# Optimization experiments

Measured on AMD Instinct MI355X. Metric: run time of the kernel, lower is better.

Reference implementation:

```python
import jax, jax.numpy as jnp
import numpy as np

N_NODES = 40000
N_EDGES = 640000
D_IN = 128
D_HID = 128
D_OUT = 128


def _glorot(key, shape):
    fan_in, fan_out = shape[1], shape[0]
    lim = np.sqrt(6.0 / (fan_in + fan_out))
    return jax.random.uniform(key, shape, jnp.float32, -lim, lim)


def setup_inputs() -> dict:
    key = jax.random.key(0)
    ks = jax.random.split(key, 8)
    x = jax.random.normal(ks[0], (N_NODES, D_IN), jnp.float32)
    edge_index = jax.random.randint(ks[1], (2, N_EDGES), 0, N_NODES, jnp.int64)
    return {
        "x": x,
        "edge_index": edge_index,
        # layer 1 (SAGEConv -> hidden): lin_l (neighbor branch, with bias), lin_r (root, no bias)
        "W1_l": _glorot(ks[2], (D_HID, D_IN)),
        "b1_l": jnp.zeros((D_HID,), jnp.float32),
        "W1_r": _glorot(ks[3], (D_HID, D_IN)),
        # layer 2 (SAGEConv -> out)
        "W2_l": _glorot(ks[4], (D_OUT, D_HID)),
        "b2_l": jnp.zeros((D_OUT,), jnp.float32),
        "W2_r": _glorot(ks[5], (D_OUT, D_HID)),
    }


def _sage_conv(x, src, dst, W_l, b_l, W_r, n_nodes):
    # mean aggregation of source features at destination nodes
    msg_sum = jax.ops.segment_sum(x[src], dst, num_segments=n_nodes)  # [N, D]
    deg = jax.ops.segment_sum(jnp.ones((src.shape[0],), x.dtype), dst,
                              num_segments=n_nodes)  # [N]
    mean = msg_sum / jnp.maximum(deg, 1.0)[:, None]  # zero for isolated nodes
    return mean @ W_l.T + b_l + x @ W_r.T


def reference(x, edge_index, W1_l, b1_l, W1_r, W2_l, b2_l, W2_r):
    src, dst = edge_index[0], edge_index[1]
    n = x.shape[0]
    h = _sage_conv(x, src, dst, W1_l, b1_l, W1_r, n)
    h = jax.nn.relu(h)
    out = _sage_conv(h, src, dst, W2_l, b2_l, W2_r, n)
    return out
```

## Files before the change

### kernel.cpp

```cpp
#include <hip/hip_runtime.h>

#define N_NODES 40000
#define N_EDGES 640000
#define D 128
#define ELLW 48
#define SENT 40000

typedef __attribute__((ext_vector_type(8))) short short8;
typedef __attribute__((ext_vector_type(4))) float f32x4;
typedef __attribute__((ext_vector_type(2))) float f32x2;

__device__ __forceinline__ unsigned short f2bf(float f) {
  unsigned int u = __float_as_uint(f);
  u += 0x7fffu + ((u >> 16) & 1u);
  return (unsigned short)(u >> 16);
}
__device__ __forceinline__ float bflo(unsigned int v) { return __uint_as_float(v << 16); }
__device__ __forceinline__ float bfhi(unsigned int v) { return __uint_as_float(v & 0xffff0000u); }

__device__ __forceinline__ unsigned int pk_fp8x4(float a, float b, float c, float d) {
  int v = __builtin_amdgcn_cvt_pk_fp8_f32(a, b, 0, false);
  v = __builtin_amdgcn_cvt_pk_fp8_f32(c, d, v, true);
  return (unsigned int)v;
}
__device__ __forceinline__ void acc_fp8x4(unsigned int u, float* a) {
  f32x2 p0 = __builtin_amdgcn_cvt_pk_f32_fp8(u, false);
  f32x2 p1 = __builtin_amdgcn_cvt_pk_f32_fp8(u, true);
  a[0] += p0[0]; a[1] += p0[1]; a[2] += p1[0]; a[3] += p1[1];
}

__global__ void k_prep(const float* __restrict__ x, unsigned short* __restrict__ xb,
                       unsigned short* __restrict__ hb,
                       unsigned char* __restrict__ xf8, unsigned char* __restrict__ hf8,
                       int* __restrict__ deg, unsigned short* __restrict__ ell,
                       const float* __restrict__ w0, const float* __restrict__ w1,
                       const float* __restrict__ w2, const float* __restrict__ w3,
                       unsigned short* __restrict__ o0, unsigned short* __restrict__ o1,
                       unsigned short* __restrict__ o2, unsigned short* __restrict__ o3) {
  int b = blockIdx.x;
  int tid = threadIdx.x;
  if (b < 5000) {
    int i = b * 256 + tid;
    if (i < N_NODES / 4) ((int4*)deg)[i] = make_int4(0, 0, 0, 0);
    float4 v = ((const float4*)x)[i];
    unsigned int lo = (unsigned int)f2bf(v.x) | ((unsigned int)f2bf(v.y) << 16);
    unsigned int hi = (unsigned int)f2bf(v.z) | ((unsigned int)f2bf(v.w) << 16);
    ((uint2*)xb)[i] = make_uint2(lo, hi);
    ((unsigned int*)xf8)[i] = pk_fp8x4(v.x, v.y, v.z, v.w);
  } else if (b < 5064) {
    if (b == 5000) {
      if (tid < 64) {
        ((unsigned int*)(xb + (size_t)SENT * D))[tid] = 0u;
        ((unsigned int*)(hb + (size_t)SENT * D))[tid] = 0u;
      } else if (tid < 96) {
        ((unsigned int*)(xf8 + (size_t)SENT * D))[tid - 64] = 0u;
      } else if (tid < 128) {
        ((unsigned int*)(hf8 + (size_t)SENT * D))[tid - 96] = 0u;
      }
    }
    int i = (b - 5000) * 256 + tid;
    int m = i >> 12, j = i & 4095;
    const float* s = (m == 0) ? w0 : (m == 1) ? w1 : (m == 2) ? w2 : w3;
    unsigned short* o = (m == 0) ? o0 : (m == 1) ? o1 : (m == 2) ? o2 : o3;
    float4 v = ((const float4*)s)[j];
    unsigned int lo = (unsigned int)f2bf(v.x) | ((unsigned int)f2bf(v.y) << 16);
    unsigned int hi = (unsigned int)f2bf(v.z) | ((unsigned int)f2bf(v.w) << 16);
    ((uint2*)o)[j] = make_uint2(lo, hi);
  } else {
    int i = (b - 5064) * 256 + tid;
    if (i < N_NODES * ELLW / 8) {
      unsigned int sv = (SENT & 0xffffu) | ((unsigned int)SENT << 16);
      uint4 q; q.x = sv; q.y = sv; q.z = sv; q.w = sv;
      ((uint4*)ell)[i] = q;
    }
  }
}

__global__ void k_fillell(const int* __restrict__ src, const int* __restrict__ dst,
                          int* __restrict__ deg, unsigned short* __restrict__ ell) {
  int e = blockIdx.x * 256 + threadIdx.x;
  if (e < N_EDGES) {
    int d = dst[e];
    int pos = atomicAdd(&deg[d], 1);
    if (pos < ELLW) ell[(size_t)d * ELLW + pos] = (unsigned short)src[e];
  }
}

__global__ void k_agg(const uint4* __restrict__ t8, const int* __restrict__ deg,
                      const unsigned short* __restrict__ ell, uint4* __restrict__ mean4) {
  int node = blockIdx.x * 32 + (threadIdx.x >> 3);
  int s = threadIdx.x & 7;
  int d = deg[node];
  int cnt = d < ELLW ? d : ELLW;
  int cntp = (cnt + 3) & ~3;
  const unsigned short* row = ell + (size_t)node * ELLW;
  float a[16];
#pragma unroll
  for (int i = 0; i < 16; ++i) a[i] = 0.f;
  for (int e = 0; e < cntp; e += 4) {
    int i0 = row[e], i1 = row[e + 1], i2 = row[e + 2], i3 = row[e + 3];
    uint4 v0 = t8[(size_t)i0 * 8 + s];
    uint4 v1 = t8[(size_t)i1 * 8 + s];
    uint4 v2 = t8[(size_t)i2 * 8 + s];
    uint4 v3 = t8[(size_t)i3 * 8 + s];
    acc_fp8x4(v0.x, a + 0); acc_fp8x4(v0.y, a + 4);
    acc_fp8x4(v0.z, a + 8); acc_fp8x4(v0.w, a + 12);
    acc_fp8x4(v1.x, a + 0); acc_fp8x4(v1.y, a + 4);
    acc_fp8x4(v1.z, a + 8); acc_fp8x4(v1.w, a + 12);
    acc_fp8x4(v2.x, a + 0); acc_fp8x4(v2.y, a + 4);
    acc_fp8x4(v2.z, a + 8); acc_fp8x4(v2.w, a + 12);
    acc_fp8x4(v3.x, a + 0); acc_fp8x4(v3.y, a + 4);
    acc_fp8x4(v3.z, a + 8); acc_fp8x4(v3.w, a + 12);
  }
  float inv = 1.0f / (float)(d > 1 ? d : 1);
#pragma unroll
  for (int i = 0; i < 16; ++i) a[i] *= inv;
  uint4 o0, o1;
  o0.x = (unsigned int)f2bf(a[0]) | ((unsigned int)f2bf(a[1]) << 16);
  o0.y = (unsigned int)f2bf(a[2]) | ((unsigned int)f2bf(a[3]) << 16);
  o0.z = (unsigned int)f2bf(a[4]) | ((unsigned int)f2bf(a[5]) << 16);
  o0.w = (unsigned int)f2bf(a[6]) | ((unsigned int)f2bf(a[7]) << 16);
  o1.x = (unsigned int)f2bf(a[8]) | ((unsigned int)f2bf(a[9]) << 16);
  o1.y = (unsigned int)f2bf(a[10]) | ((unsigned int)f2bf(a[11]) << 16);
  o1.z = (unsigned int)f2bf(a[12]) | ((unsigned int)f2bf(a[13]) << 16);
  o1.w = (unsigned int)f2bf(a[14]) | ((unsigned int)f2bf(a[15]) << 16);
  mean4[(size_t)node * 16 + s * 2] = o0;
  mean4[(size_t)node * 16 + s * 2 + 1] = o1;
}

__global__ __launch_bounds__(64) void k_gemm(
    const unsigned short* __restrict__ Al, const unsigned short* __restrict__ Ar,
    const unsigned short* __restrict__ Wl, const unsigned short* __restrict__ Wr,
    const float* __restrict__ bias,
    unsigned short* __restrict__ out_bf, unsigned char* __restrict__ out_f8,
    float* __restrict__ out_f, int relu_bf16) {
  const int lane = threadIdx.x;
  const int m0 = blockIdx.x * 32;
  const int ml = lane & 15;
  const int kg = lane >> 4;
  const unsigned short* al0 = Al + (size_t)(m0 + ml) * 128 + kg * 8;
  const unsigned short* ar0 = Ar + (size_t)(m0 + ml) * 128 + kg * 8;
  const unsigned short* al1 = al0 + 16 * 128;
  const unsigned short* ar1 = ar0 + 16 * 128;
  const unsigned short* wl_p = Wl + (size_t)ml * 128 + kg * 8;
  const unsigned short* wr_p = Wr + (size_t)ml * 128 + kg * 8;

  f32x4 acc[2][8];
#pragma unroll
  for (int mt = 0; mt < 2; ++mt)
#pragma unroll
    for (int nt = 0; nt < 8; ++nt) acc[mt][nt] = 0;

#pragma unroll
  for (int kt = 0; kt < 4; ++kt) {
    short8 a0l = *(const short8*)(al0 + kt * 32);
    short8 a0r = *(const short8*)(ar0 + kt * 32);
    short8 a1l = *(const short8*)(al1 + kt * 32);
    short8 a1r = *(const short8*)(ar1 + kt * 32);
#pragma unroll
    for (int nt = 0; nt < 8; ++nt) {
      short8 b_l = *(const short8*)(wl_p + nt * 2048 + kt * 32);
      short8 b_r = *(const short8*)(wr_p + nt * 2048 + kt * 32);
      acc[0][nt] = __builtin_amdgcn_mfma_f32_16x16x32_bf16(a0l, b_l, acc[0][nt], 0, 0, 0);
      acc[0][nt] = __builtin_amdgcn_mfma_f32_16x16x32_bf16(a0r, b_r, acc[0][nt], 0, 0, 0);
      acc[1][nt] = __builtin_amdgcn_mfma_f32_16x16x32_bf16(a1l, b_l, acc[1][nt], 0, 0, 0);
      acc[1][nt] = __builtin_amdgcn_mfma_f32_16x16x32_bf16(a1r, b_r, acc[1][nt], 0, 0, 0);
    }
  }

#pragma unroll
  for (int mt = 0; mt < 2; ++mt) {
    const int orow = m0 + mt * 16 + kg * 4;
#pragma unroll
    for (int nt = 0; nt < 8; ++nt) {
      int col = nt * 16 + ml;
      float b = bias[col];
#pragma unroll
      for (int r = 0; r < 4; ++r) {
        float o = acc[mt][nt][r] + b;
        if (relu_bf16) {
          o = fmaxf(o, 0.f);
          out_bf[(size_t)(orow + r) * 128 + col] = f2bf(o);
          unsigned int p8 = (unsigned int)__builtin_amdgcn_cvt_pk_fp8_f32(o, o, 0, false);
          out_f8[(size_t)(orow + r) * 128 + col] = (unsigned char)(p8 & 0xffu);
        } else {
          out_f[(size_t)(orow + r) * 128 + col] = o;
        }
      }
    }
  }
}

extern "C" void kernel_launch(void* const* d_in, const int* in_sizes, int n_in,
                              void* d_out, int out_size, void* d_ws, size_t ws_size,
                              hipStream_t stream) {
  const float* x   = (const float*)d_in[0];
  const int*   ei  = (const int*)d_in[1];
  const float* W1l = (const float*)d_in[2];
  const float* b1l = (const float*)d_in[3];
  const float* W1r = (const float*)d_in[4];
  const float* W2l = (const float*)d_in[5];
  const float* b2l = (const float*)d_in[6];
  const float* W2r = (const float*)d_in[7];
  const int* srcp = ei;
  const int* dstp = ei + N_EDGES;

  char* ws = (char*)d_ws;
  size_t off = 0;
  auto alloc = [&](size_t bytes) {
    void* p = ws + off;
    off = (off + bytes + 255) & ~(size_t)255;
    return p;
  };
  int* deg             = (int*)alloc((size_t)N_NODES * 4);
  unsigned short* ell  = (unsigned short*)alloc((size_t)N_NODES * ELLW * 2);
  unsigned short* w1lb = (unsigned short*)alloc((size_t)D * D * 2);
  unsigned short* w1rb = (unsigned short*)alloc((size_t)D * D * 2);
  unsigned short* w2lb = (unsigned short*)alloc((size_t)D * D * 2);
  unsigned short* w2rb = (unsigned short*)alloc((size_t)D * D * 2);
  unsigned short* xb   = (unsigned short*)alloc((size_t)(N_NODES + 1) * D * 2);
  unsigned short* mb   = (unsigned short*)alloc((size_t)N_NODES * D * 2);
  unsigned short* hb   = (unsigned short*)alloc((size_t)(N_NODES + 1) * D * 2);
  unsigned char* xf8   = (unsigned char*)alloc((size_t)(N_NODES + 1) * D);
  unsigned char* hf8   = (unsigned char*)alloc((size_t)(N_NODES + 1) * D);

  k_prep<<<6002, 256, 0, stream>>>(x, xb, hb, xf8, hf8, deg, ell,
                                   W1l, W1r, W2l, W2r, w1lb, w1rb, w2lb, w2rb);

  k_fillell<<<(N_EDGES + 255) / 256, 256, 0, stream>>>(srcp, dstp, deg, ell);

  k_agg<<<N_NODES / 32, 256, 0, stream>>>((const uint4*)xf8, deg, ell, (uint4*)mb);
  k_gemm<<<N_NODES / 32, 64, 0, stream>>>(mb, xb, w1lb, w1rb, b1l, hb, hf8, nullptr, 1);

  k_agg<<<N_NODES / 32, 256, 0, stream>>>((const uint4*)hf8, deg, ell, (uint4*)mb);
  k_gemm<<<N_NODES / 32, 64, 0, stream>>>(mb, hb, w2lb, w2rb, b2l, nullptr, nullptr,
                                          (float*)d_out, 0);
}
```

Before: 106.1 us.

## Fuse neighbor aggregation and GEMM into one per-layer kernel via LDS

Merges the aggregation kernel and the MFMA GEMM kernel into a single k_layer kernel per SAGE layer. The mean features now go through a swizzled shared-memory tile instead of a global bf16 buffer, which removes a global write/read round trip and one launch per layer. The GEMM work is split across 4 waves, each owning two 16-column output tiles. The gather loop now loads 8 ELL indices at once with a vector load and unrolls by 8, which raises memory-level parallelism but pads rows to multiples of 8 with sentinel gathers.

```diff
diff --git a/kernel.cpp b/kernel.cpp
--- a/kernel.cpp
+++ b/kernel.cpp
@@ -15,8 +15,6 @@
   u += 0x7fffu + ((u >> 16) & 1u);
   return (unsigned short)(u >> 16);
 }
-__device__ __forceinline__ float bflo(unsigned int v) { return __uint_as_float(v << 16); }
-__device__ __forceinline__ float bfhi(unsigned int v) { return __uint_as_float(v & 0xffff0000u); }
 
 __device__ __forceinline__ unsigned int pk_fp8x4(float a, float b, float c, float d) {
   int v = __builtin_amdgcn_cvt_pk_fp8_f32(a, b, 0, false);
@@ -86,98 +84,118 @@
   }
 }
 
-__global__ void k_agg(const uint4* __restrict__ t8, const int* __restrict__ deg,
-                      const unsigned short* __restrict__ ell, uint4* __restrict__ mean4) {
-  int node = blockIdx.x * 32 + (threadIdx.x >> 3);
-  int s = threadIdx.x & 7;
-  int d = deg[node];
-  int cnt = d < ELLW ? d : ELLW;
-  int cntp = (cnt + 3) & ~3;
-  const unsigned short* row = ell + (size_t)node * ELLW;
-  float a[16];
-#pragma unroll
-  for (int i = 0; i < 16; ++i) a[i] = 0.f;
-  for (int e = 0; e < cntp; e += 4) {
-    int i0 = row[e], i1 = row[e + 1], i2 = row[e + 2], i3 = row[e + 3];
-    uint4 v0 = t8[(size_t)i0 * 8 + s];
-    uint4 v1 = t8[(size_t)i1 * 8 + s];
-    uint4 v2 = t8[(size_t)i2 * 8 + s];
-    uint4 v3 = t8[(size_t)i3 * 8 + s];
-    acc_fp8x4(v0.x, a + 0); acc_fp8x4(v0.y, a + 4);
-    acc_fp8x4(v0.z, a + 8); acc_fp8x4(v0.w, a + 12);
-    acc_fp8x4(v1.x, a + 0); acc_fp8x4(v1.y, a + 4);
-    acc_fp8x4(v1.z, a + 8); acc_fp8x4(v1.w, a + 12);
-    acc_fp8x4(v2.x, a + 0); acc_fp8x4(v2.y, a + 4);
-    acc_fp8x4(v2.z, a + 8); acc_fp8x4(v2.w, a + 12);
-    acc_fp8x4(v3.x, a + 0); acc_fp8x4(v3.y, a + 4);
-    acc_fp8x4(v3.z, a + 8); acc_fp8x4(v3.w, a + 12);
-  }
-  float inv = 1.0f / (float)(d > 1 ? d : 1);
-#pragma unroll
-  for (int i = 0; i < 16; ++i) a[i] *= inv;
-  uint4 o0, o1;
-  o0.x = (unsigned int)f2bf(a[0]) | ((unsigned int)f2bf(a[1]) << 16);
-  o0.y = (unsigned int)f2bf(a[2]) | ((unsigned int)f2bf(a[3]) << 16);
-  o0.z = (unsigned int)f2bf(a[4]) | ((unsigned int)f2bf(a[5]) << 16);
-  o0.w = (unsigned int)f2bf(a[6]) | ((unsigned int)f2bf(a[7]) << 16);
-  o1.x = (unsigned int)f2bf(a[8]) | ((unsigned int)f2bf(a[9]) << 16);
-  o1.y = (unsigned int)f2bf(a[10]) | ((unsigned int)f2bf(a[11]) << 16);
-  o1.z = (unsigned int)f2bf(a[12]) | ((unsigned int)f2bf(a[13]) << 16);
-  o1.w = (unsigned int)f2bf(a[14]) | ((unsigned int)f2bf(a[15]) << 16);
-  mean4[(size_t)node * 16 + s * 2] = o0;
-  mean4[(size_t)node * 16 + s * 2 + 1] = o1;
-}
-
-__global__ __launch_bounds__(64) void k_gemm(
-    const unsigned short* __restrict__ Al, const unsigned short* __restrict__ Ar,
+__global__ __launch_bounds__(256) void k_layer(
+    const uint4* __restrict__ t8,
+    const unsigned short* __restrict__ featb,
+    const int* __restrict__ deg, const unsigned short* __restrict__ ell,
     const unsigned short* __restrict__ Wl, const unsigned short* __restrict__ Wr,
     const float* __restrict__ bias,
     unsigned short* __restrict__ out_bf, unsigned char* __restrict__ out_f8,
     float* __restrict__ out_f, int relu_bf16) {
-  const int lane = threadIdx.x;
+  __shared__ uint4 sM[32 * 16];
+  const int tid = threadIdx.x;
   const int m0 = blockIdx.x * 32;
+
+  {
+    int nloc = tid >> 3;
+    int node = m0 + nloc;
+    int s = tid & 7;
+    int d = deg[node];
+    int cnt = d < ELLW ? d : ELLW;
+    int cntp = (cnt + 7) & ~7;
+    const unsigned short* row = ell + (size_t)node * ELLW;
+    float a[16];
+#pragma unroll
+    for (int i = 0; i < 16; ++i) a[i] = 0.f;
+    for (int e = 0; e < cntp; e += 8) {
+      uint4 iv = *(const uint4*)(row + e);
+      int i0 = iv.x & 0xffff, i1 = iv.x >> 16;
+      int i2 = iv.y & 0xffff, i3 = iv.y >> 16;
+      int i4 = iv.z & 0xffff, i5 = iv.z >> 16;
+      int i6 = iv.w & 0xffff, i7 = iv.w >> 16;
+      uint4 v0 = t8[(size_t)i0 * 8 + s];
+      uint4 v1 = t8[(size_t)i1 * 8 + s];
+      uint4 v2 = t8[(size_t)i2 * 8 + s];
+      uint4 v3 = t8[(size_t)i3 * 8 + s];
+      uint4 v4 = t8[(size_t)i4 * 8 + s];
+      uint4 v5 = t8[(size_t)i5 * 8 + s];
+      uint4 v6 = t8[(size_t)i6 * 8 + s];
+      uint4 v7 = t8[(size_t)i7 * 8 + s];
+      acc_fp8x4(v0.x, a + 0); acc_fp8x4(v0.y, a + 4); acc_fp8x4(v0.z, a + 8); acc_fp8x4(v0.w, a + 12);
+      acc_fp8x4(v1.x, a + 0); acc_fp8x4(v1.y, a + 4); acc_fp8x4(v1.z, a + 8); acc_fp8x4(v1.w, a + 12);
+      acc_fp8x4(v2.x, a + 0); acc_fp8x4(v2.y, a + 4); acc_fp8x4(v2.z, a + 8); acc_fp8x4(v2.w, a + 12);
+      acc_fp8x4(v3.x, a + 0); acc_fp8x4(v3.y, a + 4); acc_fp8x4(v3.z, a + 8); acc_fp8x4(v3.w, a + 12);
+      acc_fp8x4(v4.x, a + 0); acc_fp8x4(v4.y, a + 4); acc_fp8x4(v4.z, a + 8); acc_fp8x4(v4.w, a + 12);
+      acc_fp8x4(v5.x, a + 0); acc_fp8x4(v5.y, a + 4); acc_fp8x4(v5.z, a + 8); acc_fp8x4(v5.w, a + 12);
+      acc_fp8x4(v6.x, a + 0); acc_fp8x4(v6.y, a + 4); acc_fp8x4(v6.z, a + 8); acc_fp8x4(v6.w, a + 12);
+      acc_fp8x4(v7.x, a + 0); acc_fp8x4(v7.y, a + 4); acc_fp8x4(v7.z, a + 8); acc_fp8x4(v7.w, a + 12);
+    }
+    float inv = 1.0f / (float)(d > 1 ? d : 1);
+#pragma unroll
+    for (int i = 0; i < 16; ++i) a[i] *= inv;
+    uint4 o0, o1;
+    o0.x = (unsigned int)f2bf(a[0]) | ((unsigned int)f2bf(a[1]) << 16);
+    o0.y = (unsigned int)f2bf(a[2]) | ((unsigned int)f2bf(a[3]) << 16);
+    o0.z = (unsigned int)f2bf(a[4]) | ((unsigned int)f2bf(a[5]) << 16);
+    o0.w = (unsigned int)f2bf(a[6]) | ((unsigned int)f2bf(a[7]) << 16);
+    o1.x = (unsigned int)f2bf(a[8]) | ((unsigned int)f2bf(a[9]) << 16);
+    o1.y = (unsigned int)f2bf(a[10]) | ((unsigned int)f2bf(a[11]) << 16);
+    o1.z = (unsigned int)f2bf(a[12]) | ((unsigned int)f2bf(a[13]) << 16);
+    o1.w = (unsigned int)f2bf(a[14]) | ((unsigned int)f2bf(a[15]) << 16);
+    int c0 = 2 * s, c1 = 2 * s + 1;
+    sM[nloc * 16 + (c0 ^ (nloc & 7))] = o0;
+    sM[nloc * 16 + (c1 ^ (nloc & 7))] = o1;
+  }
+  __syncthreads();
+
+  const int wid = tid >> 6, lane = tid & 63;
   const int ml = lane & 15;
   const int kg = lane >> 4;
-  const unsigned short* al0 = Al + (size_t)(m0 + ml) * 128 + kg * 8;
-  const unsigned short* ar0 = Ar + (size_t)(m0 + ml) * 128 + kg * 8;
-  const unsigned short* al1 = al0 + 16 * 128;
+  const unsigned short* ar0 = featb + (size_t)(m0 + ml) * 128 + kg * 8;
   const unsigned short* ar1 = ar0 + 16 * 128;
-  const unsigned short* wl_p = Wl + (size_t)ml * 128 + kg * 8;
-  const unsigned short* wr_p = Wr + (size_t)ml * 128 + kg * 8;
-
-  f32x4 acc[2][8];
+  const int nt0 = wid * 2, nt1 = wid * 2 + 1;
+  const unsigned short* wl0 = Wl + (size_t)(nt0 * 16 + ml) * 128 + kg * 8;
+  const unsigned short* wl1 = Wl + (size_t)(nt1 * 16 + ml) * 128 + kg * 8;
+  const unsigned short* wr0 = Wr + (size_t)(nt0 * 16 + ml) * 128 + kg * 8;
+  const unsigned short* wr1 = Wr + (size_t)(nt1 * 16 + ml) * 128 + kg * 8;
+
+  f32x4 acc[2][2];
 #pragma unroll
   for (int mt = 0; mt < 2; ++mt)
 #pragma unroll
-    for (int nt = 0; nt < 8; ++nt) acc[mt][nt] = 0;
+    for (int t = 0; t < 2; ++t) acc[mt][t] = 0;
 
 #pragma unroll
   for (int kt = 0; kt < 4; ++kt) {
-    short8 a0l = *(const short8*)(al0 + kt * 32);
+    int c = kt * 4 + kg;
+    short8 a0l = *(const short8*)&sM[ml * 16 + (c ^ (ml & 7))];
+    short8 a1l = *(const short8*)&sM[(16 + ml) * 16 + (c ^ (ml & 7))];
     short8 a0r = *(const short8*)(ar0 + kt * 32);
-    short8 a1l = *(const short8*)(al1 + kt * 32);
     short8 a1r = *(const short8*)(ar1 + kt * 32);
-#pragma unroll
-    for (int nt = 0; nt < 8; ++nt) {
-      short8 b_l = *(const short8*)(wl_p + nt * 2048 + kt * 32);
-      short8 b_r = *(const short8*)(wr_p + nt * 2048 + kt * 32);
-      acc[0][nt] = __builtin_amdgcn_mfma_f32_16x16x32_bf16(a0l, b_l, acc[0][nt], 0, 0, 0);
-      acc[0][nt] = __builtin_amdgcn_mfma_f32_16x16x32_bf16(a0r, b_r, acc[0][nt], 0, 0, 0);
-      acc[1][nt] = __builtin_amdgcn_mfma_f32_16x16x32_bf16(a1l, b_l, acc[1][nt], 0, 0, 0);
-      acc[1][nt] = __builtin_amdgcn_mfma_f32_16x16x32_bf16(a1r, b_r, acc[1][nt], 0, 0, 0);
-    }
+    short8 bl0 = *(const short8*)(wl0 + kt * 32);
+    short8 br0 = *(const short8*)(wr0 + kt * 32);
+    short8 bl1 = *(const short8*)(wl1 + kt * 32);
+    short8 br1 = *(const short8*)(wr1 + kt * 32);
+    acc[0][0] = __builtin_amdgcn_mfma_f32_16x16x32_bf16(a0l, bl0, acc[0][0], 0, 0, 0);
+    acc[0][0] = __builtin_amdgcn_mfma_f32_16x16x32_bf16(a0r, br0, acc[0][0], 0, 0, 0);
+    acc[1][0] = __builtin_amdgcn_mfma_f32_16x16x32_bf16(a1l, bl0, acc[1][0], 0, 0, 0);
+    acc[1][0] = __builtin_amdgcn_mfma_f32_16x16x32_bf16(a1r, br0, acc[1][0], 0, 0, 0);
+    acc[0][1] = __builtin_amdgcn_mfma_f32_16x16x32_bf16(a0l, bl1, acc[0][1], 0, 0, 0);
+    acc[0][1] = __builtin_amdgcn_mfma_f32_16x16x32_bf16(a0r, br1, acc[0][1], 0, 0, 0);
+    acc[1][1] = __builtin_amdgcn_mfma_f32_16x16x32_bf16(a1l, bl1, acc[1][1], 0, 0, 0);
+    acc[1][1] = __builtin_amdgcn_mfma_f32_16x16x32_bf16(a1r, br1, acc[1][1], 0, 0, 0);
   }
 
 #pragma unroll
   for (int mt = 0; mt < 2; ++mt) {
     const int orow = m0 + mt * 16 + kg * 4;
 #pragma unroll
-    for (int nt = 0; nt < 8; ++nt) {
-      int col = nt * 16 + ml;
+    for (int t = 0; t < 2; ++t) {
+      int col = (wid * 2 + t) * 16 + ml;
       float b = bias[col];
 #pragma unroll
       for (int r = 0; r < 4; ++r) {
-        float o = acc[mt][nt][r] + b;
+        float o = acc[mt][t][r] + b;
         if (relu_bf16) {
           o = fmaxf(o, 0.f);
           out_bf[(size_t)(orow + r) * 128 + col] = f2bf(o);
@@ -219,7 +237,6 @@
   unsigned short* w2lb = (unsigned short*)alloc((size_t)D * D * 2);
   unsigned short* w2rb = (unsigned short*)alloc((size_t)D * D * 2);
   unsigned short* xb   = (unsigned short*)alloc((size_t)(N_NODES + 1) * D * 2);
-  unsigned short* mb   = (unsigned short*)alloc((size_t)N_NODES * D * 2);
   unsigned short* hb   = (unsigned short*)alloc((size_t)(N_NODES + 1) * D * 2);
   unsigned char* xf8   = (unsigned char*)alloc((size_t)(N_NODES + 1) * D);
   unsigned char* hf8   = (unsigned char*)alloc((size_t)(N_NODES + 1) * D);
@@ -229,10 +246,9 @@
 
   k_fillell<<<(N_EDGES + 255) / 256, 256, 0, stream>>>(srcp, dstp, deg, ell);
 
-  k_agg<<<N_NODES / 32, 256, 0, stream>>>((const uint4*)xf8, deg, ell, (uint4*)mb);
-  k_gemm<<<N_NODES / 32, 64, 0, stream>>>(mb, xb, w1lb, w1rb, b1l, hb, hf8, nullptr, 1);
-
-  k_agg<<<N_NODES / 32, 256, 0, stream>>>((const uint4*)hf8, deg, ell, (uint4*)mb);
-  k_gemm<<<N_NODES / 32, 64, 0, stream>>>(mb, hb, w2lb, w2rb, b2l, nullptr, nullptr,
-                                          (float*)d_out, 0);
-}
+  k_layer<<<N_NODES / 32, 256, 0, stream>>>((const uint4*)xf8, xb, deg, ell,
+                                            w1lb, w1rb, b1l, hb, hf8, nullptr, 1);
+  k_layer<<<N_NODES / 32, 256, 0, stream>>>((const uint4*)hf8, hb, deg, ell,
+                                            w2lb, w2rb, b2l, nullptr, nullptr,
+                                            (float*)d_out, 0);
+}
```

Result: slower. 111.7 us (+5.3%).

## Fuse x bf16 conversion into layer-1 GEMM and widen ELL index loads

Applied to the files above, without the earlier changes.

Removes the separate bf16 copy of x written in the prep kernel; the first GEMM now reads fp32 x directly and converts to bf16 in registers. This drops one full write and re-read of a 10MB buffer at the cost of reading 20MB fp32 in the GEMM. Separately, the aggregation loop now loads 8 ELL indices with one 16-byte vector load and issues 8 gathers per iteration instead of 4. The padding to multiples of 8 relies on ELLW=48 being divisible by 8 and on sentinel-filled slots.

```diff
diff --git a/kernel.cpp b/kernel.cpp
--- a/kernel.cpp
+++ b/kernel.cpp
@@ -15,8 +15,6 @@
   u += 0x7fffu + ((u >> 16) & 1u);
   return (unsigned short)(u >> 16);
 }
-__device__ __forceinline__ float bflo(unsigned int v) { return __uint_as_float(v << 16); }
-__device__ __forceinline__ float bfhi(unsigned int v) { return __uint_as_float(v & 0xffff0000u); }
 
 __device__ __forceinline__ unsigned int pk_fp8x4(float a, float b, float c, float d) {
   int v = __builtin_amdgcn_cvt_pk_fp8_f32(a, b, 0, false);
@@ -28,9 +26,18 @@
   f32x2 p1 = __builtin_amdgcn_cvt_pk_f32_fp8(u, true);
   a[0] += p0[0]; a[1] += p0[1]; a[2] += p1[0]; a[3] += p1[1];
 }
-
-__global__ void k_prep(const float* __restrict__ x, unsigned short* __restrict__ xb,
-                       unsigned short* __restrict__ hb,
+__device__ __forceinline__ short8 ld8_f32_bf16(const float* p) {
+  float4 v0 = *(const float4*)p;
+  float4 v1 = *(const float4*)(p + 4);
+  short8 r;
+  r[0] = (short)f2bf(v0.x); r[1] = (short)f2bf(v0.y);
+  r[2] = (short)f2bf(v0.z); r[3] = (short)f2bf(v0.w);
+  r[4] = (short)f2bf(v1.x); r[5] = (short)f2bf(v1.y);
+  r[6] = (short)f2bf(v1.z); r[7] = (short)f2bf(v1.w);
+  return r;
+}
+
+__global__ void k_prep(const float* __restrict__ x,
                        unsigned char* __restrict__ xf8, unsigned char* __restrict__ hf8,
                        int* __restrict__ deg, unsigned short* __restrict__ ell,
                        const float* __restrict__ w0, const float* __restrict__ w1,
@@ -43,20 +50,11 @@
     int i = b * 256 + tid;
     if (i < N_NODES / 4) ((int4*)deg)[i] = make_int4(0, 0, 0, 0);
     float4 v = ((const float4*)x)[i];
-    unsigned int lo = (unsigned int)f2bf(v.x) | ((unsigned int)f2bf(v.y) << 16);
-    unsigned int hi = (unsigned int)f2bf(v.z) | ((unsigned int)f2bf(v.w) << 16);
-    ((uint2*)xb)[i] = make_uint2(lo, hi);
     ((unsigned int*)xf8)[i] = pk_fp8x4(v.x, v.y, v.z, v.w);
   } else if (b < 5064) {
-    if (b == 5000) {
-      if (tid < 64) {
-        ((unsigned int*)(xb + (size_t)SENT * D))[tid] = 0u;
-        ((unsigned int*)(hb + (size_t)SENT * D))[tid] = 0u;
-      } else if (tid < 96) {
-        ((unsigned int*)(xf8 + (size_t)SENT * D))[tid - 64] = 0u;
-      } else if (tid < 128) {
-        ((unsigned int*)(hf8 + (size_t)SENT * D))[tid - 96] = 0u;
-      }
+    if (b == 5000 && tid < 64) {
+      if (tid < 32) ((unsigned int*)(xf8 + (size_t)SENT * D))[tid] = 0u;
+      else          ((unsigned int*)(hf8 + (size_t)SENT * D))[tid - 32] = 0u;
     }
     int i = (b - 5000) * 256 + tid;
     int m = i >> 12, j = i & 4095;
@@ -92,25 +90,33 @@
   int s = threadIdx.x & 7;
   int d = deg[node];
   int cnt = d < ELLW ? d : ELLW;
-  int cntp = (cnt + 3) & ~3;
+  int cntp = (cnt + 7) & ~7;
   const unsigned short* row = ell + (size_t)node * ELLW;
   float a[16];
 #pragma unroll
   for (int i = 0; i < 16; ++i) a[i] = 0.f;
-  for (int e = 0; e < cntp; e += 4) {
-    int i0 = row[e], i1 = row[e + 1], i2 = row[e + 2], i3 = row[e + 3];
+  for (int e = 0; e < cntp; e += 8) {
+    uint4 iv = *(const uint4*)(row + e);
+    int i0 = iv.x & 0xffff, i1 = iv.x >> 16;
+    int i2 = iv.y & 0xffff, i3 = iv.y >> 16;
+    int i4 = iv.z & 0xffff, i5 = iv.z >> 16;
+    int i6 = iv.w & 0xffff, i7 = iv.w >> 16;
     uint4 v0 = t8[(size_t)i0 * 8 + s];
     uint4 v1 = t8[(size_t)i1 * 8 + s];
     uint4 v2 = t8[(size_t)i2 * 8 + s];
     uint4 v3 = t8[(size_t)i3 * 8 + s];
-    acc_fp8x4(v0.x, a + 0); acc_fp8x4(v0.y, a + 4);
-    acc_fp8x4(v0.z, a + 8); acc_fp8x4(v0.w, a + 12);
-    acc_fp8x4(v1.x, a + 0); acc_fp8x4(v1.y, a + 4);
-    acc_fp8x4(v1.z, a + 8); acc_fp8x4(v1.w, a + 12);
-    acc_fp8x4(v2.x, a + 0); acc_fp8x4(v2.y, a + 4);
-    acc_fp8x4(v2.z, a + 8); acc_fp8x4(v2.w, a + 12);
-    acc_fp8x4(v3.x, a + 0); acc_fp8x4(v3.y, a + 4);
-    acc_fp8x4(v3.z, a + 8); acc_fp8x4(v3.w, a + 12);
+    uint4 v4 = t8[(size_t)i4 * 8 + s];
+    uint4 v5 = t8[(size_t)i5 * 8 + s];
+    uint4 v6 = t8[(size_t)i6 * 8 + s];
+    uint4 v7 = t8[(size_t)i7 * 8 + s];
+    acc_fp8x4(v0.x, a + 0); acc_fp8x4(v0.y, a + 4); acc_fp8x4(v0.z, a + 8); acc_fp8x4(v0.w, a + 12);
+    acc_fp8x4(v1.x, a + 0); acc_fp8x4(v1.y, a + 4); acc_fp8x4(v1.z, a + 8); acc_fp8x4(v1.w, a + 12);
+    acc_fp8x4(v2.x, a + 0); acc_fp8x4(v2.y, a + 4); acc_fp8x4(v2.z, a + 8); acc_fp8x4(v2.w, a + 12);
+    acc_fp8x4(v3.x, a + 0); acc_fp8x4(v3.y, a + 4); acc_fp8x4(v3.z, a + 8); acc_fp8x4(v3.w, a + 12);
+    acc_fp8x4(v4.x, a + 0); acc_fp8x4(v4.y, a + 4); acc_fp8x4(v4.z, a + 8); acc_fp8x4(v4.w, a + 12);
+    acc_fp8x4(v5.x, a + 0); acc_fp8x4(v5.y, a + 4); acc_fp8x4(v5.z, a + 8); acc_fp8x4(v5.w, a + 12);
+    acc_fp8x4(v6.x, a + 0); acc_fp8x4(v6.y, a + 4); acc_fp8x4(v6.z, a + 8); acc_fp8x4(v6.w, a + 12);
+    acc_fp8x4(v7.x, a + 0); acc_fp8x4(v7.y, a + 4); acc_fp8x4(v7.z, a + 8); acc_fp8x4(v7.w, a + 12);
   }
   float inv = 1.0f / (float)(d > 1 ? d : 1);
 #pragma unroll
@@ -129,7 +135,8 @@
 }
 
 __global__ __launch_bounds__(64) void k_gemm(
-    const unsigned short* __restrict__ Al, const unsigned short* __restrict__ Ar,
+    const unsigned short* __restrict__ Al,
+    const unsigned short* __restrict__ Ar_bf, const float* __restrict__ Ar_f32,
     const unsigned short* __restrict__ Wl, const unsigned short* __restrict__ Wr,
     const float* __restrict__ bias,
     unsigned short* __restrict__ out_bf, unsigned char* __restrict__ out_f8,
@@ -139,9 +146,6 @@
   const int ml = lane & 15;
   const int kg = lane >> 4;
   const unsigned short* al0 = Al + (size_t)(m0 + ml) * 128 + kg * 8;
-  const unsigned short* ar0 = Ar + (size_t)(m0 + ml) * 128 + kg * 8;
-  const unsigned short* al1 = al0 + 16 * 128;
-  const unsigned short* ar1 = ar0 + 16 * 128;
   const unsigned short* wl_p = Wl + (size_t)ml * 128 + kg * 8;
   const unsigned short* wr_p = Wr + (size_t)ml * 128 + kg * 8;
 
@@ -154,9 +158,15 @@
 #pragma unroll
   for (int kt = 0; kt < 4; ++kt) {
     short8 a0l = *(const short8*)(al0 + kt * 32);
-    short8 a0r = *(const short8*)(ar0 + kt * 32);
-    short8 a1l = *(const short8*)(al1 + kt * 32);
-    short8 a1r = *(const short8*)(ar1 + kt * 32);
+    short8 a1l = *(const short8*)(al0 + 16 * 128 + kt * 32);
+    short8 a0r, a1r;
+    if (Ar_f32) {
+      a0r = ld8_f32_bf16(Ar_f32 + (size_t)(m0 + ml) * 128 + kg * 8 + kt * 32);
+      a1r = ld8_f32_bf16(Ar_f32 + (size_t)(m0 + 16 + ml) * 128 + kg * 8 + kt * 32);
+    } else {
+      a0r = *(const short8*)(Ar_bf + (size_t)(m0 + ml) * 128 + kg * 8 + kt * 32);
+      a1r = *(const short8*)(Ar_bf + (size_t)(m0 + 16 + ml) * 128 + kg * 8 + kt * 32);
+    }
 #pragma unroll
     for (int nt = 0; nt < 8; ++nt) {
       short8 b_l = *(const short8*)(wl_p + nt * 2048 + kt * 32);
@@ -218,21 +228,21 @@
   unsigned short* w1rb = (unsigned short*)alloc((size_t)D * D * 2);
   unsigned short* w2lb = (unsigned short*)alloc((size_t)D * D * 2);
   unsigned short* w2rb = (unsigned short*)alloc((size_t)D * D * 2);
-  unsigned short* xb   = (unsigned short*)alloc((size_t)(N_NODES + 1) * D * 2);
   unsigned short* mb   = (unsigned short*)alloc((size_t)N_NODES * D * 2);
-  unsigned short* hb   = (unsigned short*)alloc((size_t)(N_NODES + 1) * D * 2);
+  unsigned short* hb   = (unsigned short*)alloc((size_t)N_NODES * D * 2);
   unsigned char* xf8   = (unsigned char*)alloc((size_t)(N_NODES + 1) * D);
   unsigned char* hf8   = (unsigned char*)alloc((size_t)(N_NODES + 1) * D);
 
-  k_prep<<<6002, 256, 0, stream>>>(x, xb, hb, xf8, hf8, deg, ell,
+  k_prep<<<6002, 256, 0, stream>>>(x, xf8, hf8, deg, ell,
                                    W1l, W1r, W2l, W2r, w1lb, w1rb, w2lb, w2rb);
 
   k_fillell<<<(N_EDGES + 255) / 256, 256, 0, stream>>>(srcp, dstp, deg, ell);
 
   k_agg<<<N_NODES / 32, 256, 0, stream>>>((const uint4*)xf8, deg, ell, (uint4*)mb);
-  k_gemm<<<N_NODES / 32, 64, 0, stream>>>(mb, xb, w1lb, w1rb, b1l, hb, hf8, nullptr, 1);
+  k_gemm<<<N_NODES / 32, 64, 0, stream>>>(mb, nullptr, x, w1lb, w1rb, b1l,
+                                          hb, hf8, nullptr, 1);
 
   k_agg<<<N_NODES / 32, 256, 0, stream>>>((const uint4*)hf8, deg, ell, (uint4*)mb);
-  k_gemm<<<N_NODES / 32, 64, 0, stream>>>(mb, hb, w2lb, w2rb, b2l, nullptr, nullptr,
-                                          (float*)d_out, 0);
-}
+  k_gemm<<<N_NODES / 32, 64, 0, stream>>>(mb, hb, nullptr, w2lb, w2rb, b2l,
+                                          nullptr, nullptr, (float*)d_out, 0);
+}
```

Measured after the change: 164.7 us. 1.55x slower.
